# Optimization experiments

Hardware: AMD Instinct MI355X
Metric: run time of the kernel (lower is better)

## Reference

```python
import jax, jax.numpy as jnp
import numpy as np

OBS_LEN = 20
IN_DIM = 64
HID_DIM = 128
BATCH = 65536


def setup_inputs() -> dict:
    key = jax.random.key(0)
    ks = jax.random.split(key, 9)
    s_emb = 1.0 / np.sqrt(2.0)
    s_lstm = 1.0 / np.sqrt(HID_DIM)
    return {
        "obs_goal": jax.random.normal(ks[0], (OBS_LEN, BATCH, 2), dtype=jnp.float32),
        "h0": jax.random.normal(ks[1], (BATCH, HID_DIM), dtype=jnp.float32),
        "c0": jax.random.normal(ks[2], (BATCH, HID_DIM), dtype=jnp.float32),
        "W_emb": jax.random.uniform(ks[3], (IN_DIM, 2), jnp.float32, -s_emb, s_emb),
        "b_emb": jax.random.uniform(ks[4], (IN_DIM,), jnp.float32, -s_emb, s_emb),
        "W_ih": jax.random.uniform(ks[5], (4 * HID_DIM, IN_DIM), jnp.float32, -s_lstm, s_lstm),
        "W_hh": jax.random.uniform(ks[6], (4 * HID_DIM, HID_DIM), jnp.float32, -s_lstm, s_lstm),
        "b_ih": jax.random.uniform(ks[7], (4 * HID_DIM,), jnp.float32, -s_lstm, s_lstm),
        "b_hh": jax.random.uniform(ks[8], (4 * HID_DIM,), jnp.float32, -s_lstm, s_lstm),
    }


def reference(obs_goal, h0, c0, W_emb, b_emb, W_ih, W_hh, b_ih, b_hh):
    # input embedding: [T*B, 2] @ [2, D] -> [T, B, D]
    T, B, _ = obs_goal.shape
    x_emb = (obs_goal.reshape(-1, 2) @ W_emb.T + b_emb).reshape(T, B, IN_DIM)

    def step(carry, x_t):
        h, c = carry
        # gates: [B, 4H], torch LSTMCell chunk order = (i, f, g, o)
        gates = x_t @ W_ih.T + b_ih + h @ W_hh.T + b_hh
        i, f, g, o = jnp.split(gates, 4, axis=-1)
        i = jax.nn.sigmoid(i)
        f = jax.nn.sigmoid(f)
        g = jnp.tanh(g)
        o = jax.nn.sigmoid(o)
        c_new = f * c + i * g
        h_new = o * jnp.tanh(c_new)
        return (h_new, c_new), None

    (h_final, _), _ = jax.lax.scan(step, (h0, c0), x_emb[:OBS_LEN])
    return h_final
```

## Files before the change

kernel.cpp:

```cpp
#include <hip/hip_runtime.h>

#define OBS_T 20
#define HID 128
#define NGATE 512
#define MB 16
#define HSTR 136

typedef __bf16 bf16x8 __attribute__((ext_vector_type(8)));
typedef __bf16 bf16x4 __attribute__((ext_vector_type(4)));
typedef float f32x4 __attribute__((ext_vector_type(4)));
typedef float f32x2 __attribute__((ext_vector_type(2)));

__device__ __forceinline__ float fast_rcp(float x) { return __builtin_amdgcn_rcpf(x); }
#if __has_builtin(__builtin_amdgcn_exp2f)
__device__ __forceinline__ float exp2_hw(float x) { return __builtin_amdgcn_exp2f(x); }
#else
__device__ __forceinline__ float exp2_hw(float x) { return __expf(x * 0.69314718056f); }
#endif
#define LOG2E 1.442695041f

__device__ __host__ __forceinline__ float gate_scale(int q) {
  return (q == 2) ? (-2.0f * LOG2E) : (-LOG2E);
}

__global__ void prep_vec(const float* __restrict__ W_emb, const float* __restrict__ b_emb,
                         const float* __restrict__ W_ih, const float* __restrict__ b_ih,
                         const float* __restrict__ b_hh,
                         float* __restrict__ biasp, float* __restrict__ wx0p,
                         float* __restrict__ wx1p) {
  int r = blockIdx.x * blockDim.x + threadIdx.x;
  if (r >= NGATE) return;
  float s0 = 0.f, s1 = 0.f, sb = 0.f;
  for (int d = 0; d < 64; ++d) {
    float w = W_ih[r * 64 + d];
    s0 += w * W_emb[d * 2 + 0];
    s1 += w * W_emb[d * 2 + 1];
    sb += w * b_emb[d];
  }
  int q = r >> 7, j = r & 127;
  float sc = gate_scale(q);
  int np = (j >> 4) * 64 + q * 16 + (j & 15);
  biasp[np] = (b_ih[r] + b_hh[r] + sb) * sc;
  wx0p[np] = s0 * sc;
  wx1p[np] = s1 * sc;
}

__global__ void prep_wp(const float* __restrict__ W_hh, __bf16* __restrict__ Wp) {
  int tid = blockIdx.x * blockDim.x + threadIdx.x;
  int jj = tid & 7;
  int lane = (tid >> 3) & 63;
  int frag = tid >> 9;
  int ks = frag & 3;
  int q = (frag >> 2) & 3;
  int g16 = frag >> 4;
  int cn = lane & 15, quad = lane >> 4;
  int r = q * 128 + g16 * 16 + cn;
  int k = ks * 32 + quad * 8 + jj;
  Wp[tid] = (__bf16)(W_hh[r * 128 + k] * gate_scale(q));
}

__device__ __forceinline__ f32x2 exp2_2(f32x2 v) {
  f32x2 r;
  r.x = exp2_hw(v.x);
  r.y = exp2_hw(v.y);
  return r;
}
__device__ __forceinline__ f32x2 rcp_2(f32x2 v) {
  f32x2 r;
  r.x = fast_rcp(v.x);
  r.y = fast_rcp(v.y);
  return r;
}

__device__ __forceinline__ f32x2 cell_update_pk(f32x2 gi, f32x2 gf, f32x2 gg,
                                                f32x2 go, f32x2& c) {
  f32x2 e_i = exp2_2(gi);
  f32x2 e_f = exp2_2(gf);
  f32x2 e_g = exp2_2(gg);
  f32x2 e_o = exp2_2(go);
  f32x2 a_i = e_i + 1.f;
  f32x2 a_f = e_f + 1.f;
  f32x2 a_g = e_g + 1.f;
  f32x2 bg = 1.f - e_g;
  f32x2 m1 = a_i * a_g;
  f32x2 r = rcp_2(m1 * a_f);
  f32x2 t = c * m1 + bg * a_f;
  c = t * r;
  f32x2 e_c = exp2_2(c * (-2.f * LOG2E));
  f32x2 a_c = e_c + 1.f;
  f32x2 bc = 1.f - e_c;
  return bc * rcp_2((e_o + 1.f) * a_c);
}

__global__ __launch_bounds__(512, 4) void lstm_fused(
    const float* __restrict__ obs, const float* __restrict__ h0,
    const float* __restrict__ c0, const __bf16* __restrict__ Wp,
    const float* __restrict__ biasp, const float* __restrict__ wx0p,
    const float* __restrict__ wx1p, float* __restrict__ out, int batch) {
  __shared__ __align__(16) __bf16 hbuf[2][MB][HSTR];
  __shared__ __align__(16) float obs_s[OBS_T][MB][2];
  __shared__ __align__(16) float wx0_s[NGATE];
  __shared__ __align__(16) float wx1_s[NGATE];

  const int tid = threadIdx.x;
  const int lane = tid & 63;
  const int wv = tid >> 6;
  const int cn = lane & 15;
  const int quad = lane >> 4;
  const int bbase = blockIdx.x * MB;
  const int ju = wv * 16 + cn;

  if (tid < OBS_T * MB * 2 / 4) {
    const int t = tid >> 3, f4 = tid & 7;
    ((float4*)obs_s)[tid] = ((const float4*)obs)[(t * batch + bbase) / 2 + f4];
  }
  wx0_s[tid] = wx0p[tid];
  wx1_s[tid] = wx1p[tid];
  {
    int row = tid >> 5, c4 = tid & 31;
    float4 v = ((const float4*)h0)[(bbase + row) * 32 + c4];
    bf16x4 b;
    b.x = (__bf16)v.x; b.y = (__bf16)v.y; b.z = (__bf16)v.z; b.w = (__bf16)v.w;
    *(bf16x4*)&hbuf[0][row][c4 * 4] = b;
  }

  bf16x8 Bf[4][4];
  {
    const bf16x8* wp8 = (const bf16x8*)Wp;
#pragma unroll
    for (int q = 0; q < 4; ++q)
#pragma unroll
      for (int ks = 0; ks < 4; ++ks)
        Bf[ks][q] = wp8[(wv * 16 + q * 4 + ks) * 64 + lane];
  }

  float bias_v[4];
#pragma unroll
  for (int q = 0; q < 4; ++q)
    bias_v[q] = biasp[wv * 64 + q * 16 + cn];

  f32x2 cc2[2];
#pragma unroll
  for (int p = 0; p < 2; ++p) {
    cc2[p].x = c0[(bbase + quad * 4 + 2 * p + 0) * HID + ju];
    cc2[p].y = c0[(bbase + quad * 4 + 2 * p + 1) * HID + ju];
  }

  __syncthreads();

  int cur = 0;
#pragma unroll 1
  for (int t = 0; t < OBS_T - 1; ++t) {
    f32x4 acc[4];
#pragma unroll
    for (int q = 0; q < 4; ++q) {
      int n = wv * 64 + q * 16 + cn;
      float w0q = wx0_s[n], w1q = wx1_s[n];
#pragma unroll
      for (int r = 0; r < 4; ++r) {
        float2 ob = *(const float2*)&obs_s[t][quad * 4 + r][0];
        acc[q][r] = fmaf(ob.y, w1q, fmaf(ob.x, w0q, bias_v[q]));
      }
    }

#pragma unroll
    for (int ks = 0; ks < 4; ++ks) {
      bf16x8 Av = *(const bf16x8*)&hbuf[cur][cn][ks * 32 + quad * 8];
#pragma unroll
      for (int q = 0; q < 4; ++q)
        acc[q] = __builtin_amdgcn_mfma_f32_16x16x32_bf16(Av, Bf[ks][q], acc[q], 0, 0, 0);
    }

    const int nxt = cur ^ 1;
    {
      f32x2 hlo = cell_update_pk(acc[0].xy, acc[1].xy, acc[2].xy, acc[3].xy, cc2[0]);
      f32x2 hhi = cell_update_pk(acc[0].zw, acc[1].zw, acc[2].zw, acc[3].zw, cc2[1]);
      hbuf[nxt][quad * 4 + 0][ju] = (__bf16)hlo.x;
      hbuf[nxt][quad * 4 + 1][ju] = (__bf16)hlo.y;
      hbuf[nxt][quad * 4 + 2][ju] = (__bf16)hhi.x;
      hbuf[nxt][quad * 4 + 3][ju] = (__bf16)hhi.y;
    }
    __syncthreads();
    cur = nxt;
  }

  {
    const int t = OBS_T - 1;
    f32x4 acc[4];
#pragma unroll
    for (int q = 0; q < 4; ++q) {
      int n = wv * 64 + q * 16 + cn;
      float w0q = wx0_s[n], w1q = wx1_s[n];
#pragma unroll
      for (int r = 0; r < 4; ++r) {
        float2 ob = *(const float2*)&obs_s[t][quad * 4 + r][0];
        acc[q][r] = fmaf(ob.y, w1q, fmaf(ob.x, w0q, bias_v[q]));
      }
    }
#pragma unroll
    for (int ks = 0; ks < 4; ++ks) {
      bf16x8 Av = *(const bf16x8*)&hbuf[cur][cn][ks * 32 + quad * 8];
#pragma unroll
      for (int q = 0; q < 4; ++q)
        acc[q] = __builtin_amdgcn_mfma_f32_16x16x32_bf16(Av, Bf[ks][q], acc[q], 0, 0, 0);
    }
    {
      f32x2 hlo = cell_update_pk(acc[0].xy, acc[1].xy, acc[2].xy, acc[3].xy, cc2[0]);
      f32x2 hhi = cell_update_pk(acc[0].zw, acc[1].zw, acc[2].zw, acc[3].zw, cc2[1]);
      out[(bbase + quad * 4 + 0) * HID + ju] = hlo.x;
      out[(bbase + quad * 4 + 1) * HID + ju] = hlo.y;
      out[(bbase + quad * 4 + 2) * HID + ju] = hhi.x;
      out[(bbase + quad * 4 + 3) * HID + ju] = hhi.y;
    }
  }
}

extern "C" void kernel_launch(void* const* d_in, const int* in_sizes, int n_in,
                              void* d_out, int out_size, void* d_ws, size_t ws_size,
                              hipStream_t stream) {
  const float* obs = (const float*)d_in[0];
  const float* h0 = (const float*)d_in[1];
  const float* c0 = (const float*)d_in[2];
  const float* W_emb = (const float*)d_in[3];
  const float* b_emb = (const float*)d_in[4];
  const float* W_ih = (const float*)d_in[5];
  const float* W_hh = (const float*)d_in[6];
  const float* b_ih = (const float*)d_in[7];
  const float* b_hh = (const float*)d_in[8];
  float* out = (float*)d_out;
  const int batch = in_sizes[1] / HID;

  __bf16* Wp = (__bf16*)d_ws;
  float* biasp = (float*)((char*)d_ws + 131072);
  float* wx0p = biasp + NGATE;
  float* wx1p = wx0p + NGATE;

  prep_vec<<<2, 256, 0, stream>>>(W_emb, b_emb, W_ih, b_ih, b_hh, biasp, wx0p, wx1p);
  prep_wp<<<256, 256, 0, stream>>>(W_hh, Wp);
  lstm_fused<<<batch / MB, 512, 0, stream>>>(obs, h0, c0, Wp, biasp, wx0p, wx1p, out, batch);
}
```

Measured before the change: 348.9 us.

## Process two batch tiles per block to reuse register-resident weights

```diff
diff --git a/kernel.cpp b/kernel.cpp
--- a/kernel.cpp
+++ b/kernel.cpp
@@ -4,6 +4,7 @@
 #define HID 128
 #define NGATE 512
 #define MB 16
+#define NTILE 2
 #define HSTR 136
 
 typedef __bf16 bf16x8 __attribute__((ext_vector_type(8)));
@@ -92,36 +93,38 @@
   return bc * rcp_2((e_o + 1.f) * a_c);
 }
 
-__global__ __launch_bounds__(512, 4) void lstm_fused(
+__global__ __launch_bounds__(512, 2) void lstm_fused(
     const float* __restrict__ obs, const float* __restrict__ h0,
     const float* __restrict__ c0, const __bf16* __restrict__ Wp,
     const float* __restrict__ biasp, const float* __restrict__ wx0p,
     const float* __restrict__ wx1p, float* __restrict__ out, int batch) {
-  __shared__ __align__(16) __bf16 hbuf[2][MB][HSTR];
-  __shared__ __align__(16) float obs_s[OBS_T][MB][2];
-  __shared__ __align__(16) float wx0_s[NGATE];
-  __shared__ __align__(16) float wx1_s[NGATE];
+  __shared__ __align__(16) __bf16 hbuf[NTILE][2][MB][HSTR];
+  __shared__ __align__(16) float obs_s[NTILE][OBS_T][MB][2];
 
   const int tid = threadIdx.x;
   const int lane = tid & 63;
   const int wv = tid >> 6;
   const int cn = lane & 15;
   const int quad = lane >> 4;
-  const int bbase = blockIdx.x * MB;
+  const int bbase = blockIdx.x * (MB * NTILE);
   const int ju = wv * 16 + cn;
 
-  if (tid < OBS_T * MB * 2 / 4) {
-    const int t = tid >> 3, f4 = tid & 7;
-    ((float4*)obs_s)[tid] = ((const float4*)obs)[(t * batch + bbase) / 2 + f4];
-  }
-  wx0_s[tid] = wx0p[tid];
-  wx1_s[tid] = wx1p[tid];
+  if (tid < 2 * 160) {
+    const int tl = (tid >= 160) ? 1 : 0;
+    const int w = tid - tl * 160;
+    const int t = w >> 3, f4 = w & 7;
+    ((float4*)&obs_s[tl][0][0][0])[w] =
+        ((const float4*)obs)[(t * batch + bbase + tl * MB) / 2 + f4];
+  }
   {
-    int row = tid >> 5, c4 = tid & 31;
-    float4 v = ((const float4*)h0)[(bbase + row) * 32 + c4];
-    bf16x4 b;
-    b.x = (__bf16)v.x; b.y = (__bf16)v.y; b.z = (__bf16)v.z; b.w = (__bf16)v.w;
-    *(bf16x4*)&hbuf[0][row][c4 * 4] = b;
+    const int row = tid >> 5, c4 = tid & 31;
+#pragma unroll
+    for (int tl = 0; tl < NTILE; ++tl) {
+      float4 v = ((const float4*)h0)[(bbase + tl * MB + row) * 32 + c4];
+      bf16x4 b;
+      b.x = (__bf16)v.x; b.y = (__bf16)v.y; b.z = (__bf16)v.z; b.w = (__bf16)v.w;
+      *(bf16x4*)&hbuf[tl][0][row][c4 * 4] = b;
+    }
   }
 
   bf16x8 Bf[4][4];
@@ -134,51 +137,62 @@
         Bf[ks][q] = wp8[(wv * 16 + q * 4 + ks) * 64 + lane];
   }
 
-  float bias_v[4];
-#pragma unroll
-  for (int q = 0; q < 4; ++q)
-    bias_v[q] = biasp[wv * 64 + q * 16 + cn];
-
-  f32x2 cc2[2];
-#pragma unroll
-  for (int p = 0; p < 2; ++p) {
-    cc2[p].x = c0[(bbase + quad * 4 + 2 * p + 0) * HID + ju];
-    cc2[p].y = c0[(bbase + quad * 4 + 2 * p + 1) * HID + ju];
-  }
+  float bias_v[4], w0r[4], w1r[4];
+#pragma unroll
+  for (int q = 0; q < 4; ++q) {
+    int n = wv * 64 + q * 16 + cn;
+    bias_v[q] = biasp[n];
+    w0r[q] = wx0p[n];
+    w1r[q] = wx1p[n];
+  }
+
+  f32x2 cc2[NTILE][2];
+#pragma unroll
+  for (int tl = 0; tl < NTILE; ++tl)
+#pragma unroll
+    for (int p = 0; p < 2; ++p) {
+      cc2[tl][p].x = c0[(bbase + tl * MB + quad * 4 + 2 * p + 0) * HID + ju];
+      cc2[tl][p].y = c0[(bbase + tl * MB + quad * 4 + 2 * p + 1) * HID + ju];
+    }
 
   __syncthreads();
 
   int cur = 0;
 #pragma unroll 1
   for (int t = 0; t < OBS_T - 1; ++t) {
-    f32x4 acc[4];
-#pragma unroll
-    for (int q = 0; q < 4; ++q) {
-      int n = wv * 64 + q * 16 + cn;
-      float w0q = wx0_s[n], w1q = wx1_s[n];
-#pragma unroll
-      for (int r = 0; r < 4; ++r) {
-        float2 ob = *(const float2*)&obs_s[t][quad * 4 + r][0];
-        acc[q][r] = fmaf(ob.y, w1q, fmaf(ob.x, w0q, bias_v[q]));
-      }
-    }
-
-#pragma unroll
-    for (int ks = 0; ks < 4; ++ks) {
-      bf16x8 Av = *(const bf16x8*)&hbuf[cur][cn][ks * 32 + quad * 8];
-#pragma unroll
-      for (int q = 0; q < 4; ++q)
-        acc[q] = __builtin_amdgcn_mfma_f32_16x16x32_bf16(Av, Bf[ks][q], acc[q], 0, 0, 0);
+    f32x4 acc[NTILE][4];
+#pragma unroll
+    for (int tl = 0; tl < NTILE; ++tl) {
+#pragma unroll
+      for (int q = 0; q < 4; ++q) {
+        float w0q = w0r[q], w1q = w1r[q];
+#pragma unroll
+        for (int r = 0; r < 4; ++r) {
+          float2 ob = *(const float2*)&obs_s[tl][t][quad * 4 + r][0];
+          acc[tl][q][r] = fmaf(ob.y, w1q, fmaf(ob.x, w0q, bias_v[q]));
+        }
+      }
+#pragma unroll
+      for (int ks = 0; ks < 4; ++ks) {
+        bf16x8 Av = *(const bf16x8*)&hbuf[tl][cur][cn][ks * 32 + quad * 8];
+#pragma unroll
+        for (int q = 0; q < 4; ++q)
+          acc[tl][q] = __builtin_amdgcn_mfma_f32_16x16x32_bf16(Av, Bf[ks][q],
+                                                               acc[tl][q], 0, 0, 0);
+      }
     }
 
     const int nxt = cur ^ 1;
-    {
-      f32x2 hlo = cell_update_pk(acc[0].xy, acc[1].xy, acc[2].xy, acc[3].xy, cc2[0]);
-      f32x2 hhi = cell_update_pk(acc[0].zw, acc[1].zw, acc[2].zw, acc[3].zw, cc2[1]);
-      hbuf[nxt][quad * 4 + 0][ju] = (__bf16)hlo.x;
-      hbuf[nxt][quad * 4 + 1][ju] = (__bf16)hlo.y;
-      hbuf[nxt][quad * 4 + 2][ju] = (__bf16)hhi.x;
-      hbuf[nxt][quad * 4 + 3][ju] = (__bf16)hhi.y;
+#pragma unroll
+    for (int tl = 0; tl < NTILE; ++tl) {
+      f32x2 hlo = cell_update_pk(acc[tl][0].xy, acc[tl][1].xy, acc[tl][2].xy,
+                                 acc[tl][3].xy, cc2[tl][0]);
+      f32x2 hhi = cell_update_pk(acc[tl][0].zw, acc[tl][1].zw, acc[tl][2].zw,
+                                 acc[tl][3].zw, cc2[tl][1]);
+      hbuf[tl][nxt][quad * 4 + 0][ju] = (__bf16)hlo.x;
+      hbuf[tl][nxt][quad * 4 + 1][ju] = (__bf16)hlo.y;
+      hbuf[tl][nxt][quad * 4 + 2][ju] = (__bf16)hhi.x;
+      hbuf[tl][nxt][quad * 4 + 3][ju] = (__bf16)hhi.y;
     }
     __syncthreads();
     cur = nxt;
@@ -186,31 +200,38 @@
 
   {
     const int t = OBS_T - 1;
-    f32x4 acc[4];
-#pragma unroll
-    for (int q = 0; q < 4; ++q) {
-      int n = wv * 64 + q * 16 + cn;
-      float w0q = wx0_s[n], w1q = wx1_s[n];
-#pragma unroll
-      for (int r = 0; r < 4; ++r) {
-        float2 ob = *(const float2*)&obs_s[t][quad * 4 + r][0];
-        acc[q][r] = fmaf(ob.y, w1q, fmaf(ob.x, w0q, bias_v[q]));
-      }
-    }
-#pragma unroll
-    for (int ks = 0; ks < 4; ++ks) {
-      bf16x8 Av = *(const bf16x8*)&hbuf[cur][cn][ks * 32 + quad * 8];
-#pragma unroll
-      for (int q = 0; q < 4; ++q)
-        acc[q] = __builtin_amdgcn_mfma_f32_16x16x32_bf16(Av, Bf[ks][q], acc[q], 0, 0, 0);
-    }
-    {
-      f32x2 hlo = cell_update_pk(acc[0].xy, acc[1].xy, acc[2].xy, acc[3].xy, cc2[0]);
-      f32x2 hhi = cell_update_pk(acc[0].zw, acc[1].zw, acc[2].zw, acc[3].zw, cc2[1]);
-      out[(bbase + quad * 4 + 0) * HID + ju] = hlo.x;
-      out[(bbase + quad * 4 + 1) * HID + ju] = hlo.y;
-      out[(bbase + quad * 4 + 2) * HID + ju] = hhi.x;
-      out[(bbase + quad * 4 + 3) * HID + ju] = hhi.y;
+    f32x4 acc[NTILE][4];
+#pragma unroll
+    for (int tl = 0; tl < NTILE; ++tl) {
+#pragma unroll
+      for (int q = 0; q < 4; ++q) {
+        float w0q = w0r[q], w1q = w1r[q];
+#pragma unroll
+        for (int r = 0; r < 4; ++r) {
+          float2 ob = *(const float2*)&obs_s[tl][t][quad * 4 + r][0];
+          acc[tl][q][r] = fmaf(ob.y, w1q, fmaf(ob.x, w0q, bias_v[q]));
+        }
+      }
+#pragma unroll
+      for (int ks = 0; ks < 4; ++ks) {
+        bf16x8 Av = *(const bf16x8*)&hbuf[tl][cur][cn][ks * 32 + quad * 8];
+#pragma unroll
+        for (int q = 0; q < 4; ++q)
+          acc[tl][q] = __builtin_amdgcn_mfma_f32_16x16x32_bf16(Av, Bf[ks][q],
+                                                               acc[tl][q], 0, 0, 0);
+      }
+    }
+#pragma unroll
+    for (int tl = 0; tl < NTILE; ++tl) {
+      f32x2 hlo = cell_update_pk(acc[tl][0].xy, acc[tl][1].xy, acc[tl][2].xy,
+                                 acc[tl][3].xy, cc2[tl][0]);
+      f32x2 hhi = cell_update_pk(acc[tl][0].zw, acc[tl][1].zw, acc[tl][2].zw,
+                                 acc[tl][3].zw, cc2[tl][1]);
+      const int rb = bbase + tl * MB + quad * 4;
+      out[(rb + 0) * HID + ju] = hlo.x;
+      out[(rb + 1) * HID + ju] = hlo.y;
+      out[(rb + 2) * HID + ju] = hhi.x;
+      out[(rb + 3) * HID + ju] = hhi.y;
     }
   }
 }
@@ -237,5 +258,6 @@
 
   prep_vec<<<2, 256, 0, stream>>>(W_emb, b_emb, W_ih, b_ih, b_hh, biasp, wx0p, wx1p);
   prep_wp<<<256, 256, 0, stream>>>(W_hh, Wp);
-  lstm_fused<<<batch / MB, 512, 0, stream>>>(obs, h0, c0, Wp, biasp, wx0p, wx1p, out, batch);
-}
+  lstm_fused<<<batch / (MB * NTILE), 512, 0, stream>>>(obs, h0, c0, Wp, biasp,
+                                                       wx0p, wx1p, out, batch);
+}
```

Result: slower. 366.5 us (+5.0%).
